# Kernel optimization log

Hardware: AMD Instinct MI355X
Metric: run time of the kernel (lower is better)

The kernel has to match this reference:

```python
import jax, jax.numpy as jnp
import numpy as np

N = 50000       # nodes
E = 1200000     # edges (before self-loops)
IN_CH = 128
HID = 64
L = 3           # FAConv layers
EPS_RES = 0.1   # FAConv eps residual weight
BN_EPS = 1e-5


def _bn(x, g, b):
    # BatchNorm1d, training-mode statistics (biased variance, like torch)
    mu = x.mean(axis=0)
    var = x.var(axis=0)
    return g * (x - mu) * jax.lax.rsqrt(var + BN_EPS) + b


def setup_inputs() -> dict:
    key = jax.random.key(0)
    ks = jax.random.split(key, 12)
    s = lambda d: 1.0 / np.sqrt(d)
    H2 = HID // 2
    return {
        "x": jax.random.normal(ks[0], (N, IN_CH), jnp.float32),
        "edge_index": jax.random.randint(ks[1], (2, E), 0, N, dtype=jnp.int32),
        "batch_size": 10000,
        "W_in": jax.random.normal(ks[2], (IN_CH, HID), jnp.float32) * s(IN_CH),
        "b_in": jnp.zeros((HID,), jnp.float32),
        "att_l": jax.random.normal(ks[3], (L, HID), jnp.float32) * s(HID),
        "att_r": jax.random.normal(ks[4], (L, HID), jnp.float32) * s(HID),
        "bn_g": jnp.ones((L, HID), jnp.float32),
        "bn_b": jnp.zeros((L, HID), jnp.float32),
        "W1": jax.random.normal(ks[5], (HID, HID), jnp.float32) * s(HID),
        "b1": jnp.zeros((HID,), jnp.float32),
        "g1": jnp.ones((HID,), jnp.float32),
        "be1": jnp.zeros((HID,), jnp.float32),
        "W2": jax.random.normal(ks[6], (HID, H2), jnp.float32) * s(HID),
        "b2": jnp.zeros((H2,), jnp.float32),
        "g2": jnp.ones((H2,), jnp.float32),
        "be2": jnp.zeros((H2,), jnp.float32),
        "W3": jax.random.normal(ks[7], (H2, 1), jnp.float32) * s(H2),
        "b3": jnp.zeros((1,), jnp.float32),
    }


def reference(x, edge_index, batch_size, W_in, b_in, att_l, att_r, bn_g, bn_b,
              W1, b1, g1, be1, W2, b2, g2, be2, W3, b3):
    n = x.shape[0]
    # gcn_norm with self-loops (same for all layers since graph is fixed)
    loops = jnp.arange(n, dtype=edge_index.dtype)
    src = jnp.concatenate([edge_index[0], loops])  # j (source)
    dst = jnp.concatenate([edge_index[1], loops])  # i (target)
    deg = jax.ops.segment_sum(jnp.ones_like(dst, dtype=x.dtype), dst, num_segments=n)
    dinv = jnp.where(deg > 0, jax.lax.rsqrt(deg), 0.0)
    norm = dinv[src] * dinv[dst]                   # [E+N]

    x0 = jax.nn.relu(x @ W_in + b_in)              # [N, HID]
    h = x0
    for l in range(L):
        al = h @ att_l[l]                          # [N] att_l^T x
        ar = h @ att_r[l]                          # [N] att_r^T x
        alpha = jnp.tanh(al[src] + ar[dst])        # [E+N] signed attention
        msg = h[src] * (alpha * norm)[:, None]     # gather + weight
        out = jax.ops.segment_sum(msg, dst, num_segments=n) + EPS_RES * x0
        h = _bn(jax.nn.relu(out), bn_g[l], bn_b[l])

    z = h[:batch_size]
    z = jax.nn.relu(_bn(z @ W1 + b1, g1, be1))
    z = jax.nn.relu(_bn(z @ W2 + b2, g2, be2))
    return (z @ W3 + b3).squeeze(-1)
```

## Files before the change

### kernel.cpp

```cpp
#include <hip/hip_runtime.h>
#include <hip/hip_bf16.h>
#include <math.h>

#define NND 50000
#define NE  1200000
#define TOT (NE + NND)
#define INCH 128
#define HID 64
#define H2  32
#define NL  3
#define BSZ 10000
#define NB  196
#define NHB 128
#define NSTAT 128
#define NAGG 2048
#define CHUNK 4096
#define EPS_RES 0.1f
#define BN_EPS 1e-5f

typedef unsigned short ushort8v __attribute__((ext_vector_type(8)));
typedef unsigned short ushort4v __attribute__((ext_vector_type(4)));

__device__ __forceinline__ float b2f(unsigned short u) {
    return __uint_as_float((unsigned)u << 16);
}

__device__ __forceinline__ float fast_tanh(float x) {
    float cx = fminf(fmaxf(x, -8.f), 8.f);
    float e = __expf(2.f * cx);
    return 1.f - __fdividef(2.f, e + 1.f);
}


__global__ __launch_bounds__(256) void bhist_kernel(const int* __restrict__ dst, int* __restrict__ bh_part, int ne) {
    __shared__ int arr[256];
    arr[threadIdx.x] = 0;
    __syncthreads();
    int i = blockIdx.x * 256 + threadIdx.x;
    int stride = gridDim.x * 256;
    for (int e = i; e < ne; e += stride) atomicAdd(&arr[dst[e] >> 8], 1);
    __syncthreads();
    bh_part[blockIdx.x * 256 + threadIdx.x] = arr[threadIdx.x];
}

__global__ __launch_bounds__(256) void bscan_kernel(const int* __restrict__ bh_part,
                                                    int* __restrict__ bstart, int* __restrict__ bcur,
                                                    int* __restrict__ offsets) {
    __shared__ int ls[256];
    int t = threadIdx.x;
    int v = 0;
    for (int k = 0; k < NHB; k++) v += bh_part[k * 256 + t];
    ls[t] = v;
    __syncthreads();
    for (int off = 1; off < 256; off <<= 1) {
        int tv = (t >= off) ? ls[t - off] : 0;
        __syncthreads();
        ls[t] += tv;
        __syncthreads();
    }
    int excl = ls[t] - v;
    if (t < NB) { bstart[t] = excl; bcur[t] = excl; }
    if (t == NB) bstart[NB] = ls[NB - 1];
    if (t == 0) offsets[NND] = TOT;
}

__global__ __launch_bounds__(256) void passA_kernel(const int* __restrict__ src, const int* __restrict__ dst,
                                                    int* __restrict__ bcur, unsigned* __restrict__ ebuf, int ne) {
    __shared__ int arr[256];
    int t = threadIdx.x;
    int base = blockIdx.x * CHUNK;
    int lim = min(base + CHUNK, ne);
    arr[t] = 0;
    __syncthreads();
    for (int e = base + t; e < lim; e += 256) atomicAdd(&arr[dst[e] >> 8], 1);
    __syncthreads();
    int cnt_t = arr[t];
    int claimed = 0;
    if (cnt_t > 0) claimed = atomicAdd(&bcur[t], cnt_t);
    __syncthreads();
    arr[t] = claimed;
    __syncthreads();
    for (int e = base + t; e < lim; e += 256) {
        int d = dst[e];
        int pos = atomicAdd(&arr[d >> 8], 1);
        ebuf[pos] = ((unsigned)src[e] << 8) | (unsigned)(d & 255);
    }
}

__global__ __launch_bounds__(256) void bucket_build_kernel(const unsigned* __restrict__ ebuf, const int* __restrict__ bstart,
                                                           int* __restrict__ offsets, int* __restrict__ csr,
                                                           float* __restrict__ aldi_f) {
    __shared__ int dcnt[256];
    __shared__ int ls[256];
    __shared__ int cur[256];
    int b = blockIdx.x, t = threadIdx.x;
    dcnt[t] = 0;
    __syncthreads();
    int beg = bstart[b], end = bstart[b + 1];
    for (int p = beg + t; p < end; p += 256) atomicAdd(&dcnt[ebuf[p] & 255u], 1);
    __syncthreads();
    int node = b * 256 + t;
    bool valid = node < NND;
    int d = valid ? (dcnt[t] + 1) : 0;
    ls[t] = d;
    __syncthreads();
    for (int off = 1; off < 256; off <<= 1) {
        int tv = (t >= off) ? ls[t - off] : 0;
        __syncthreads();
        ls[t] += tv;
        __syncthreads();
    }
    int off = bstart[b] + b * 256 + ls[t] - d;
    if (valid) {
        offsets[node] = off;
        aldi_f[2 * node + 1] = rsqrtf((float)d);
        csr[off] = node;
        cur[t] = off + 1;
    }
    __syncthreads();
    for (int p = beg + t; p < end; p += 256) {
        unsigned ed = ebuf[p];
        int pos = atomicAdd(&cur[ed & 255u], 1);
        csr[pos] = (int)(ed >> 8);
    }
}

__global__ __launch_bounds__(256) void gemm_in_kernel(const float* __restrict__ x, const float* __restrict__ W,
                                                      const float* __restrict__ b,
                                                      const float* __restrict__ attl, const float* __restrict__ attr,
                                                      __hip_bfloat16* __restrict__ x0bf,
                                                      float* __restrict__ aldi_f, float* __restrict__ ar) {
    __shared__ float Wl[INCH * HID];
    __shared__ float xs[16 * INCH];
    int t = threadIdx.x;
    for (int i = t; i < INCH * HID; i += 256) Wl[i] = W[i];
    size_t rowbase = (size_t)blockIdx.x * 16;
    for (int i = t; i < 16 * INCH; i += 256) xs[i] = x[rowbase * INCH + i];
    __syncthreads();
    int col = t & 63, rg = t >> 6;
    float a0 = 0.f, a1 = 0.f, a2 = 0.f, a3 = 0.f;
    for (int k = 0; k < INCH; k++) {
        float wk = Wl[k * HID + col];
        a0 = fmaf(xs[(rg * 4 + 0) * INCH + k], wk, a0);
        a1 = fmaf(xs[(rg * 4 + 1) * INCH + k], wk, a1);
        a2 = fmaf(xs[(rg * 4 + 2) * INCH + k], wk, a2);
        a3 = fmaf(xs[(rg * 4 + 3) * INCH + k], wk, a3);
    }
    float bb = b[col];
    a0 = fmaxf(a0 + bb, 0.f); a1 = fmaxf(a1 + bb, 0.f);
    a2 = fmaxf(a2 + bb, 0.f); a3 = fmaxf(a3 + bb, 0.f);
    size_t r = rowbase + rg * 4;
    x0bf[(r + 0) * HID + col] = __float2bfloat16(a0);
    x0bf[(r + 1) * HID + col] = __float2bfloat16(a1);
    x0bf[(r + 2) * HID + col] = __float2bfloat16(a2);
    x0bf[(r + 3) * HID + col] = __float2bfloat16(a3);
    float wl = attl[col], wr = attr[col];
    float p0 = a0 * wl, q0 = a0 * wr, p1 = a1 * wl, q1 = a1 * wr;
    float p2 = a2 * wl, q2 = a2 * wr, p3 = a3 * wl, q3 = a3 * wr;
    for (int off = 32; off > 0; off >>= 1) {
        p0 += __shfl_xor(p0, off); q0 += __shfl_xor(q0, off);
        p1 += __shfl_xor(p1, off); q1 += __shfl_xor(q1, off);
        p2 += __shfl_xor(p2, off); q2 += __shfl_xor(q2, off);
        p3 += __shfl_xor(p3, off); q3 += __shfl_xor(q3, off);
    }
    if (col == 0) {
        aldi_f[2 * (r + 0)] = p0; ar[r + 0] = q0;
        aldi_f[2 * (r + 1)] = p1; ar[r + 1] = q1;
        aldi_f[2 * (r + 2)] = p2; ar[r + 2] = q2;
        aldi_f[2 * (r + 3)] = p3; ar[r + 3] = q3;
    }
}

__global__ __launch_bounds__(256) void aggregate_kernel(const __hip_bfloat16* __restrict__ hbf,
                                                        const __hip_bfloat16* __restrict__ x0bf,
                                                        const float2* __restrict__ aldi,
                                                        const float* __restrict__ ar,
                                                        const int* __restrict__ offsets, const int* __restrict__ csr,
                                                        float* __restrict__ y, int n) {
    int wave = threadIdx.x >> 6;
    int lane = threadIdx.x & 63;
    int half = lane >> 5;
    int ll   = lane & 31;
    int sg   = ll >> 3;
    int cl   = (ll & 7) << 3;
    int hbase = half << 5;
    const unsigned short* hb = (const unsigned short*)hbf;
    for (int vb = blockIdx.x; (vb << 3) < n; vb += gridDim.x) {
        int v = (vb << 3) + (wave << 1) + half;
        bool vvalid = v < n;
        int beg = 0, end = 0;
        float arv = 0.f;
        if (vvalid) { beg = offsets[v]; end = offsets[v + 1]; arv = ar[v]; }
        int nstr = (end - beg + 31) >> 5;
        int mstr = max(nstr, __shfl_xor(nstr, 32));
        float a0 = 0.f, a1 = 0.f, a2 = 0.f, a3 = 0.f, a4 = 0.f, a5 = 0.f, a6 = 0.f, a7 = 0.f;
        for (int s = 0; s < mstr; ++s) {
            int sb = beg + (s << 5);
            int p = sb + ll;
            int u = 0; float c = 0.f;
            if (p < end) {
                u = csr[p];
                float2 ad = aldi[u];
                c = fast_tanh(ad.x + arv) * ad.y;
            }
            int cnt = end - sb;
            for (int ch = 0; ch < 2; ++ch) {
                int j0 = (ch << 4) + sg;
                int j1 = j0 + 4, j2 = j0 + 8, j3 = j0 + 12;
                int js0 = (j0 < cnt) ? j0 : 0;
                int js1 = (j1 < cnt) ? j1 : 0;
                int js2 = (j2 < cnt) ? j2 : 0;
                int js3 = (j3 < cnt) ? j3 : 0;
                int u0 = __shfl(u, hbase + js0); float c0 = __shfl(c, hbase + js0); if (j0 >= cnt) c0 = 0.f;
                int u1 = __shfl(u, hbase + js1); float c1 = __shfl(c, hbase + js1); if (j1 >= cnt) c1 = 0.f;
                int u2 = __shfl(u, hbase + js2); float c2 = __shfl(c, hbase + js2); if (j2 >= cnt) c2 = 0.f;
                int u3 = __shfl(u, hbase + js3); float c3 = __shfl(c, hbase + js3); if (j3 >= cnt) c3 = 0.f;
                ushort8v h0 = *(const ushort8v*)(hb + (size_t)u0 * HID + cl);
                ushort8v h1 = *(const ushort8v*)(hb + (size_t)u1 * HID + cl);
                ushort8v h2 = *(const ushort8v*)(hb + (size_t)u2 * HID + cl);
                ushort8v h3 = *(const ushort8v*)(hb + (size_t)u3 * HID + cl);
                a0 = fmaf(b2f(h0[0]), c0, a0); a1 = fmaf(b2f(h0[1]), c0, a1);
                a2 = fmaf(b2f(h0[2]), c0, a2); a3 = fmaf(b2f(h0[3]), c0, a3);
                a4 = fmaf(b2f(h0[4]), c0, a4); a5 = fmaf(b2f(h0[5]), c0, a5);
                a6 = fmaf(b2f(h0[6]), c0, a6); a7 = fmaf(b2f(h0[7]), c0, a7);
                a0 = fmaf(b2f(h1[0]), c1, a0); a1 = fmaf(b2f(h1[1]), c1, a1);
                a2 = fmaf(b2f(h1[2]), c1, a2); a3 = fmaf(b2f(h1[3]), c1, a3);
                a4 = fmaf(b2f(h1[4]), c1, a4); a5 = fmaf(b2f(h1[5]), c1, a5);
                a6 = fmaf(b2f(h1[6]), c1, a6); a7 = fmaf(b2f(h1[7]), c1, a7);
                a0 = fmaf(b2f(h2[0]), c2, a0); a1 = fmaf(b2f(h2[1]), c2, a1);
                a2 = fmaf(b2f(h2[2]), c2, a2); a3 = fmaf(b2f(h2[3]), c2, a3);
                a4 = fmaf(b2f(h2[4]), c2, a4); a5 = fmaf(b2f(h2[5]), c2, a5);
                a6 = fmaf(b2f(h2[6]), c2, a6); a7 = fmaf(b2f(h2[7]), c2, a7);
                a0 = fmaf(b2f(h3[0]), c3, a0); a1 = fmaf(b2f(h3[1]), c3, a1);
                a2 = fmaf(b2f(h3[2]), c3, a2); a3 = fmaf(b2f(h3[3]), c3, a3);
                a4 = fmaf(b2f(h3[4]), c3, a4); a5 = fmaf(b2f(h3[5]), c3, a5);
                a6 = fmaf(b2f(h3[6]), c3, a6); a7 = fmaf(b2f(h3[7]), c3, a7);
            }
        }
        for (int off = 8; off < 32; off <<= 1) {
            a0 += __shfl_xor(a0, off); a1 += __shfl_xor(a1, off);
            a2 += __shfl_xor(a2, off); a3 += __shfl_xor(a3, off);
            a4 += __shfl_xor(a4, off); a5 += __shfl_xor(a5, off);
            a6 += __shfl_xor(a6, off); a7 += __shfl_xor(a7, off);
        }
        if (sg == 0 && vvalid) {
            float dv = aldi[v].y;
            ushort8v xb = *(const ushort8v*)((const unsigned short*)x0bf + (size_t)v * HID + cl);
            float4 o0, o1;
            o0.x = fmaxf(fmaf(EPS_RES, b2f(xb[0]), a0 * dv), 0.f);
            o0.y = fmaxf(fmaf(EPS_RES, b2f(xb[1]), a1 * dv), 0.f);
            o0.z = fmaxf(fmaf(EPS_RES, b2f(xb[2]), a2 * dv), 0.f);
            o0.w = fmaxf(fmaf(EPS_RES, b2f(xb[3]), a3 * dv), 0.f);
            o1.x = fmaxf(fmaf(EPS_RES, b2f(xb[4]), a4 * dv), 0.f);
            o1.y = fmaxf(fmaf(EPS_RES, b2f(xb[5]), a5 * dv), 0.f);
            o1.z = fmaxf(fmaf(EPS_RES, b2f(xb[6]), a6 * dv), 0.f);
            o1.w = fmaxf(fmaf(EPS_RES, b2f(xb[7]), a7 * dv), 0.f);
            *(float4*)(y + (size_t)v * HID + cl) = o0;
            *(float4*)(y + (size_t)v * HID + cl + 4) = o1;
        }
    }
}

template <int C>
__global__ __launch_bounds__(256) void bn_stats_fused_kernel(const float* __restrict__ y, int rows,
                                                             const float* __restrict__ g, const float* __restrict__ b,
                                                             float rows_inv,
                                                             float* __restrict__ acc, int* __restrict__ counter,
                                                             float* __restrict__ scale, float* __restrict__ shift) {
    const int TPR = C / 4;
    const int RPW = 64 / TPR;
    int lane = threadIdx.x & 63;
    int wave = threadIdx.x >> 6;
    int cl = (lane % TPR) * 4;
    int rsub = lane / TPR;
    int rpb = 4 * RPW;
    int r = blockIdx.x * rpb + wave * RPW + rsub;
    int stride = gridDim.x * rpb;
    float s0 = 0.f, s1 = 0.f, s2 = 0.f, s3 = 0.f, q0 = 0.f, q1 = 0.f, q2 = 0.f, q3 = 0.f;
    for (; r < rows; r += stride) {
        float4 v = *(const float4*)(y + (size_t)r * C + cl);
        s0 += v.x; q0 = fmaf(v.x, v.x, q0);
        s1 += v.y; q1 = fmaf(v.y, v.y, q1);
        s2 += v.z; q2 = fmaf(v.z, v.z, q2);
        s3 += v.w; q3 = fmaf(v.w, v.w, q3);
    }
    for (int off = TPR; off < 64; off <<= 1) {
        s0 += __shfl_xor(s0, off); q0 += __shfl_xor(q0, off);
        s1 += __shfl_xor(s1, off); q1 += __shfl_xor(q1, off);
        s2 += __shfl_xor(s2, off); q2 += __shfl_xor(q2, off);
        s3 += __shfl_xor(s3, off); q3 += __shfl_xor(q3, off);
    }
    __shared__ float lsum[4][64], lsq[4][64];
    if (lane < TPR) {
        lsum[wave][cl + 0] = s0; lsq[wave][cl + 0] = q0;
        lsum[wave][cl + 1] = s1; lsq[wave][cl + 1] = q1;
        lsum[wave][cl + 2] = s2; lsq[wave][cl + 2] = q2;
        lsum[wave][cl + 3] = s3; lsq[wave][cl + 3] = q3;
    }
    __syncthreads();
    int t = threadIdx.x;
    if (t < C) {
        float ts = lsum[0][t] + lsum[1][t] + lsum[2][t] + lsum[3][t];
        float tq = lsq[0][t] + lsq[1][t] + lsq[2][t] + lsq[3][t];
        atomicAdd(&acc[t], ts);
        atomicAdd(&acc[64 + t], tq);
    }
    __shared__ int islast;
    __syncthreads();
    if (t == 0) {
        __threadfence();
        int old = atomicAdd(counter, 1);
        islast = (old == (int)gridDim.x - 1) ? 1 : 0;
    }
    __syncthreads();
    if (islast && t < C) {
        float ts = atomicAdd(&acc[t], 0.f);
        float tq = atomicAdd(&acc[64 + t], 0.f);
        float mean = ts * rows_inv;
        float var = tq * rows_inv - mean * mean;
        float sc = g[t] * rsqrtf(var + BN_EPS);
        scale[t] = sc;
        shift[t] = b[t] - mean * sc;
    }
}

__global__ __launch_bounds__(256) void bnapply_attn_kernel(const float* __restrict__ y, const float* __restrict__ scale,
                                                           const float* __restrict__ shift,
                                                           const float* __restrict__ attl, const float* __restrict__ attr,
                                                           __hip_bfloat16* __restrict__ hbf,
                                                           float* __restrict__ aldi_f, float* __restrict__ arr_out, int n) {
    int lane = threadIdx.x & 63;
    int wave = threadIdx.x >> 6;
    int rsub = lane >> 4;
    int cl = (lane & 15) << 2;
    int r = blockIdx.x * 16 + wave * 4 + rsub;
    if (r >= n) return;
    float4 v = *(const float4*)(y + (size_t)r * HID + cl);
    float4 sc = *(const float4*)(scale + cl);
    float4 sh = *(const float4*)(shift + cl);
    float v0 = fmaf(v.x, sc.x, sh.x);
    float v1 = fmaf(v.y, sc.y, sh.y);
    float v2 = fmaf(v.z, sc.z, sh.z);
    float v3 = fmaf(v.w, sc.w, sh.w);
    __hip_bfloat16 b0 = __float2bfloat16(v0), b1 = __float2bfloat16(v1);
    __hip_bfloat16 b2 = __float2bfloat16(v2), b3 = __float2bfloat16(v3);
    ushort4v hv;
    hv[0] = *(unsigned short*)&b0; hv[1] = *(unsigned short*)&b1;
    hv[2] = *(unsigned short*)&b2; hv[3] = *(unsigned short*)&b3;
    *(ushort4v*)((unsigned short*)hbf + (size_t)r * HID + cl) = hv;
    float4 wl4 = *(const float4*)(attl + cl);
    float4 wr4 = *(const float4*)(attr + cl);
    float pl = v0 * wl4.x + v1 * wl4.y + v2 * wl4.z + v3 * wl4.w;
    float pr = v0 * wr4.x + v1 * wr4.y + v2 * wr4.z + v3 * wr4.w;
    for (int off = 1; off < 16; off <<= 1) {
        pl += __shfl_xor(pl, off);
        pr += __shfl_xor(pr, off);
    }
    if ((lane & 15) == 0) { aldi_f[2 * r] = pl; arr_out[r] = pr; }
}

__global__ __launch_bounds__(256) void mlp1_kernel(const float* __restrict__ y, const float* __restrict__ scale,
                                                   const float* __restrict__ shift, const float* __restrict__ W,
                                                   const float* __restrict__ b, float* __restrict__ z1) {
    __shared__ float Wl[HID * HID];
    __shared__ float xs[16 * HID];
    int t = threadIdx.x;
    for (int i = t; i < HID * HID; i += 256) Wl[i] = W[i];
    size_t rowbase = (size_t)blockIdx.x * 16;
    for (int i = t; i < 16 * HID; i += 256) {
        int c = i & 63;
        xs[i] = fmaf(y[rowbase * HID + i], scale[c], shift[c]);
    }
    __syncthreads();
    int col = t & 63, rg = t >> 6;
    float a0 = 0.f, a1 = 0.f, a2 = 0.f, a3 = 0.f;
    for (int k = 0; k < HID; k++) {
        float wk = Wl[k * HID + col];
        a0 = fmaf(xs[(rg * 4 + 0) * HID + k], wk, a0);
        a1 = fmaf(xs[(rg * 4 + 1) * HID + k], wk, a1);
        a2 = fmaf(xs[(rg * 4 + 2) * HID + k], wk, a2);
        a3 = fmaf(xs[(rg * 4 + 3) * HID + k], wk, a3);
    }
    float bb = b[col];
    size_t r = rowbase + rg * 4;
    z1[(r + 0) * HID + col] = a0 + bb;
    z1[(r + 1) * HID + col] = a1 + bb;
    z1[(r + 2) * HID + col] = a2 + bb;
    z1[(r + 3) * HID + col] = a3 + bb;
}

__global__ __launch_bounds__(256) void mlp2_kernel(const float* __restrict__ z1, const float* __restrict__ scale,
                                                   const float* __restrict__ shift, const float* __restrict__ W,
                                                   const float* __restrict__ b, float* __restrict__ z2) {
    __shared__ float Wl[HID * H2];
    __shared__ float as[16 * HID];
    int t = threadIdx.x;
    for (int i = t; i < HID * H2; i += 256) Wl[i] = W[i];
    size_t rowbase = (size_t)blockIdx.x * 16;
    for (int i = t; i < 16 * HID; i += 256) {
        int c = i & 63;
        float v = z1[rowbase * HID + i];
        as[i] = fmaxf(fmaf(v, scale[c], shift[c]), 0.f);
    }
    __syncthreads();
    int col = t & 31, rg = t >> 5;
    float a0 = 0.f, a1 = 0.f;
    for (int k = 0; k < HID; k++) {
        float wk = Wl[k * H2 + col];
        a0 = fmaf(as[(rg * 2 + 0) * HID + k], wk, a0);
        a1 = fmaf(as[(rg * 2 + 1) * HID + k], wk, a1);
    }
    float bb = b[col];
    size_t r = rowbase + rg * 2;
    z2[(r + 0) * H2 + col] = a0 + bb;
    z2[(r + 1) * H2 + col] = a1 + bb;
}

__global__ __launch_bounds__(256) void mlp3_kernel(const float* __restrict__ z2, const float* __restrict__ scale,
                                                   const float* __restrict__ shift, const float* __restrict__ W3,
                                                   const float* __restrict__ b3, float* __restrict__ out, int rows) {
    int i = blockIdx.x * 256 + threadIdx.x;
    if (i >= rows) return;
    float acc = 0.f;
#pragma unroll
    for (int k = 0; k < H2; k++) {
        float v = fmaxf(fmaf(z2[(size_t)i * H2 + k], scale[k], shift[k]), 0.f);
        acc = fmaf(v, W3[k], acc);
    }
    out[i] = acc + b3[0];
}

extern "C" void kernel_launch(void* const* d_in, const int* in_sizes, int n_in,
                              void* d_out, int out_size, void* d_ws, size_t ws_size,
                              hipStream_t stream) {
    const float* x     = (const float*)d_in[0];
    const int*   ei    = (const int*)d_in[1];
    const int*   src   = ei;
    const int*   dst   = ei + NE;
    const float* W_in  = (const float*)d_in[3];
    const float* b_in  = (const float*)d_in[4];
    const float* att_l = (const float*)d_in[5];
    const float* att_r = (const float*)d_in[6];
    const float* bn_g  = (const float*)d_in[7];
    const float* bn_b  = (const float*)d_in[8];
    const float* W1    = (const float*)d_in[9];
    const float* b1    = (const float*)d_in[10];
    const float* g1    = (const float*)d_in[11];
    const float* be1   = (const float*)d_in[12];
    const float* W2    = (const float*)d_in[13];
    const float* b2    = (const float*)d_in[14];
    const float* g2    = (const float*)d_in[15];
    const float* be2   = (const float*)d_in[16];
    const float* W3    = (const float*)d_in[17];
    const float* b3    = (const float*)d_in[18];
    float* out = (float*)d_out;

    char* p = (char*)d_ws;
    auto carve = [&](size_t bytes) -> void* {
        void* r = (void*)p;
        p += (bytes + 255) & ~(size_t)255;
        return r;
    };
    int*   bh_part = (int*)carve((size_t)NHB * 256 * 4);
    int*   bstart  = (int*)carve(256 * 4);
    int*   bcur    = (int*)carve(256 * 4);
    int*   offsets = (int*)carve((size_t)(NND + 1) * 4);
    int*   csr     = (int*)carve((size_t)TOT * 4);
    float2* aldi   = (float2*)carve((size_t)NND * 8);
    float* ar      = (float*)carve((size_t)NND * 4);
    __hip_bfloat16* x0bf = (__hip_bfloat16*)carve((size_t)NND * HID * 2);
    __hip_bfloat16* hbfA = (__hip_bfloat16*)carve((size_t)NND * HID * 2);
    __hip_bfloat16* hbfB = (__hip_bfloat16*)carve((size_t)NND * HID * 2);
    float* ybuf    = (float*)carve((size_t)NND * HID * 4);
    unsigned* ebuf = (unsigned*)ybuf;
    float* accall  = (float*)carve(5 * 256 * 4);
    float* scale   = (float*)carve(64 * 4);
    float* shift   = (float*)carve(64 * 4);
    float* z1      = (float*)carve((size_t)BSZ * HID * 4);
    float* z2      = (float*)carve((size_t)BSZ * H2 * 4);

    auto accr = [&](int i) -> float* { return accall + i * 256; };
    auto ctr  = [&](int i) -> int*   { return (int*)(accall + i * 256 + 128); };

    const int nblkA = (NE + CHUNK - 1) / CHUNK;

    hipMemsetAsync(accall, 0, 5 * 256 * 4, stream);

    bhist_kernel<<<NHB, 256, 0, stream>>>(dst, bh_part, NE);
    gemm_in_kernel<<<NND / 16, 256, 0, stream>>>(x, W_in, b_in, att_l, att_r, x0bf, (float*)aldi, ar);
    bscan_kernel<<<1, 256, 0, stream>>>(bh_part, bstart, bcur, offsets);
    passA_kernel<<<nblkA, 256, 0, stream>>>(src, dst, bcur, ebuf, NE);
    bucket_build_kernel<<<NB, 256, 0, stream>>>(ebuf, bstart, offsets, csr, (float*)aldi);

    const __hip_bfloat16* h_in = x0bf;
    __hip_bfloat16* hbufs[2] = {hbfA, hbfB};
    for (int l = 0; l < NL; l++) {
        aggregate_kernel<<<NAGG, 256, 0, stream>>>(h_in, x0bf, aldi, ar, offsets, csr, ybuf, NND);
        bn_stats_fused_kernel<64><<<NSTAT, 256, 0, stream>>>(ybuf, NND, bn_g + l * HID, bn_b + l * HID,
                                                             1.0f / NND, accr(l), ctr(l), scale, shift);
        if (l < NL - 1) {
            bnapply_attn_kernel<<<(NND + 15) / 16, 256, 0, stream>>>(ybuf, scale, shift,
                                                                     att_l + (l + 1) * HID, att_r + (l + 1) * HID,
                                                                     hbufs[l], (float*)aldi, ar, NND);
            h_in = hbufs[l];
        }
    }

    mlp1_kernel<<<BSZ / 16, 256, 0, stream>>>(ybuf, scale, shift, W1, b1, z1);
    bn_stats_fused_kernel<64><<<NSTAT, 256, 0, stream>>>(z1, BSZ, g1, be1, 1.0f / BSZ, accr(3), ctr(3), scale, shift);

    mlp2_kernel<<<BSZ / 16, 256, 0, stream>>>(z1, scale, shift, W2, b2, z2);
    bn_stats_fused_kernel<32><<<NSTAT, 256, 0, stream>>>(z2, BSZ, g2, be2, 1.0f / BSZ, accr(4), ctr(4), scale, shift);

    mlp3_kernel<<<(BSZ + 255) / 256, 256, 0, stream>>>(z2, scale, shift, W3, b3, out, BSZ);
}
```

Before: 347.9 us.

## Fuse histogram scan into bhist and BN statistics into MLP kernels

Merges the bucket-scan kernel into the histogram kernel: global atomics accumulate the histogram and a last-block-done counter lets the final block run the scan. It also drops the two separate BN-statistics launches in the head MLP. Each MLP GEMM kernel now accumulates column sums and sums of squares with atomics, and the next kernel derives scale and shift from them. This removes three kernel launches and one re-read of z1 and z2, at the cost of global atomic contention and less precise E[x^2]-mean^2 variance.

New measurement: 357.6 us. 1.03x slower.

```diff
diff --git a/kernel.cpp b/kernel.cpp
--- a/kernel.cpp
+++ b/kernel.cpp
@@ -32,24 +32,30 @@
 }
 
 
-__global__ __launch_bounds__(256) void bhist_kernel(const int* __restrict__ dst, int* __restrict__ bh_part, int ne) {
+__global__ __launch_bounds__(256) void bhist_kernel(const int* __restrict__ dst, int* __restrict__ ghist,
+                                                    int* __restrict__ counter,
+                                                    int* __restrict__ bstart, int* __restrict__ bcur,
+                                                    int* __restrict__ offsets, int ne) {
     __shared__ int arr[256];
-    arr[threadIdx.x] = 0;
-    __syncthreads();
-    int i = blockIdx.x * 256 + threadIdx.x;
+    int t = threadIdx.x;
+    arr[t] = 0;
+    __syncthreads();
+    int i = blockIdx.x * 256 + t;
     int stride = gridDim.x * 256;
     for (int e = i; e < ne; e += stride) atomicAdd(&arr[dst[e] >> 8], 1);
     __syncthreads();
-    bh_part[blockIdx.x * 256 + threadIdx.x] = arr[threadIdx.x];
-}
-
-__global__ __launch_bounds__(256) void bscan_kernel(const int* __restrict__ bh_part,
-                                                    int* __restrict__ bstart, int* __restrict__ bcur,
-                                                    int* __restrict__ offsets) {
+    if (arr[t] > 0) atomicAdd(&ghist[t], arr[t]);
+    __shared__ int islast;
+    __syncthreads();
+    if (t == 0) {
+        __threadfence();
+        int old = atomicAdd(counter, 1);
+        islast = (old == (int)gridDim.x - 1) ? 1 : 0;
+    }
+    __syncthreads();
+    if (!islast) return;
     __shared__ int ls[256];
-    int t = threadIdx.x;
-    int v = 0;
-    for (int k = 0; k < NHB; k++) v += bh_part[k * 256 + t];
+    int v = atomicAdd(&ghist[t], 0);
     ls[t] = v;
     __syncthreads();
     for (int off = 1; off < 256; off <<= 1) {
@@ -361,9 +367,11 @@
 
 __global__ __launch_bounds__(256) void mlp1_kernel(const float* __restrict__ y, const float* __restrict__ scale,
                                                    const float* __restrict__ shift, const float* __restrict__ W,
-                                                   const float* __restrict__ b, float* __restrict__ z1) {
+                                                   const float* __restrict__ b, float* __restrict__ z1,
+                                                   float* __restrict__ acc_out) {
     __shared__ float Wl[HID * HID];
     __shared__ float xs[16 * HID];
+    __shared__ float zs[4][64], zq[4][64];
     int t = threadIdx.x;
     for (int i = t; i < HID * HID; i += 256) Wl[i] = W[i];
     size_t rowbase = (size_t)blockIdx.x * 16;
@@ -382,25 +390,48 @@
         a3 = fmaf(xs[(rg * 4 + 3) * HID + k], wk, a3);
     }
     float bb = b[col];
+    a0 += bb; a1 += bb; a2 += bb; a3 += bb;
     size_t r = rowbase + rg * 4;
-    z1[(r + 0) * HID + col] = a0 + bb;
-    z1[(r + 1) * HID + col] = a1 + bb;
-    z1[(r + 2) * HID + col] = a2 + bb;
-    z1[(r + 3) * HID + col] = a3 + bb;
-}
-
-__global__ __launch_bounds__(256) void mlp2_kernel(const float* __restrict__ z1, const float* __restrict__ scale,
-                                                   const float* __restrict__ shift, const float* __restrict__ W,
-                                                   const float* __restrict__ b, float* __restrict__ z2) {
+    z1[(r + 0) * HID + col] = a0;
+    z1[(r + 1) * HID + col] = a1;
+    z1[(r + 2) * HID + col] = a2;
+    z1[(r + 3) * HID + col] = a3;
+    zs[rg][col] = a0 + a1 + a2 + a3;
+    zq[rg][col] = a0 * a0 + a1 * a1 + a2 * a2 + a3 * a3;
+    __syncthreads();
+    if (t < 64) {
+        float s = zs[0][t] + zs[1][t] + zs[2][t] + zs[3][t];
+        float q = zq[0][t] + zq[1][t] + zq[2][t] + zq[3][t];
+        atomicAdd(&acc_out[t], s);
+        atomicAdd(&acc_out[64 + t], q);
+    }
+}
+
+__global__ __launch_bounds__(256) void mlp2_kernel(const float* __restrict__ z1,
+                                                   const float* __restrict__ acc_in, float rows_inv_in,
+                                                   const float* __restrict__ gin, const float* __restrict__ bin,
+                                                   const float* __restrict__ W, const float* __restrict__ b,
+                                                   float* __restrict__ z2, float* __restrict__ acc_out) {
     __shared__ float Wl[HID * H2];
     __shared__ float as[16 * HID];
-    int t = threadIdx.x;
+    __shared__ float s_sc[64], s_sh[64];
+    __shared__ float zs[8][32], zq[8][32];
+    int t = threadIdx.x;
+    if (t < 64) {
+        float ts = acc_in[t], tq = acc_in[64 + t];
+        float mean = ts * rows_inv_in;
+        float var = tq * rows_inv_in - mean * mean;
+        float sc = gin[t] * rsqrtf(var + BN_EPS);
+        s_sc[t] = sc;
+        s_sh[t] = bin[t] - mean * sc;
+    }
     for (int i = t; i < HID * H2; i += 256) Wl[i] = W[i];
+    __syncthreads();
     size_t rowbase = (size_t)blockIdx.x * 16;
     for (int i = t; i < 16 * HID; i += 256) {
         int c = i & 63;
         float v = z1[rowbase * HID + i];
-        as[i] = fmaxf(fmaf(v, scale[c], shift[c]), 0.f);
+        as[i] = fmaxf(fmaf(v, s_sc[c], s_sh[c]), 0.f);
     }
     __syncthreads();
     int col = t & 31, rg = t >> 5;
@@ -411,20 +442,44 @@
         a1 = fmaf(as[(rg * 2 + 1) * HID + k], wk, a1);
     }
     float bb = b[col];
+    a0 += bb; a1 += bb;
     size_t r = rowbase + rg * 2;
-    z2[(r + 0) * H2 + col] = a0 + bb;
-    z2[(r + 1) * H2 + col] = a1 + bb;
-}
-
-__global__ __launch_bounds__(256) void mlp3_kernel(const float* __restrict__ z2, const float* __restrict__ scale,
-                                                   const float* __restrict__ shift, const float* __restrict__ W3,
-                                                   const float* __restrict__ b3, float* __restrict__ out, int rows) {
-    int i = blockIdx.x * 256 + threadIdx.x;
+    z2[(r + 0) * H2 + col] = a0;
+    z2[(r + 1) * H2 + col] = a1;
+    zs[rg][col] = a0 + a1;
+    zq[rg][col] = a0 * a0 + a1 * a1;
+    __syncthreads();
+    if (t < 32) {
+        float s = 0.f, q = 0.f;
+#pragma unroll
+        for (int w = 0; w < 8; w++) { s += zs[w][t]; q += zq[w][t]; }
+        atomicAdd(&acc_out[t], s);
+        atomicAdd(&acc_out[64 + t], q);
+    }
+}
+
+__global__ __launch_bounds__(256) void mlp3_kernel(const float* __restrict__ z2,
+                                                   const float* __restrict__ acc_in, float rows_inv_in,
+                                                   const float* __restrict__ gin, const float* __restrict__ bin,
+                                                   const float* __restrict__ W3, const float* __restrict__ b3,
+                                                   float* __restrict__ out, int rows) {
+    __shared__ float s_sc[32], s_sh[32];
+    int t = threadIdx.x;
+    if (t < 32) {
+        float ts = acc_in[t], tq = acc_in[64 + t];
+        float mean = ts * rows_inv_in;
+        float var = tq * rows_inv_in - mean * mean;
+        float sc = gin[t] * rsqrtf(var + BN_EPS);
+        s_sc[t] = sc;
+        s_sh[t] = bin[t] - mean * sc;
+    }
+    __syncthreads();
+    int i = blockIdx.x * 256 + t;
     if (i >= rows) return;
     float acc = 0.f;
 #pragma unroll
     for (int k = 0; k < H2; k++) {
-        float v = fmaxf(fmaf(z2[(size_t)i * H2 + k], scale[k], shift[k]), 0.f);
+        float v = fmaxf(fmaf(z2[(size_t)i * H2 + k], s_sc[k], s_sh[k]), 0.f);
         acc = fmaf(v, W3[k], acc);
     }
     out[i] = acc + b3[0];
@@ -461,7 +516,6 @@
         p += (bytes + 255) & ~(size_t)255;
         return r;
     };
-    int*   bh_part = (int*)carve((size_t)NHB * 256 * 4);
     int*   bstart  = (int*)carve(256 * 4);
     int*   bcur    = (int*)carve(256 * 4);
     int*   offsets = (int*)carve((size_t)(NND + 1) * 4);
@@ -473,7 +527,7 @@
     __hip_bfloat16* hbfB = (__hip_bfloat16*)carve((size_t)NND * HID * 2);
     float* ybuf    = (float*)carve((size_t)NND * HID * 4);
     unsigned* ebuf = (unsigned*)ybuf;
-    float* accall  = (float*)carve(5 * 256 * 4);
+    float* accall  = (float*)carve(7 * 256 * 4);
     float* scale   = (float*)carve(64 * 4);
     float* shift   = (float*)carve(64 * 4);
     float* z1      = (float*)carve((size_t)BSZ * HID * 4);
@@ -481,14 +535,15 @@
 
     auto accr = [&](int i) -> float* { return accall + i * 256; };
     auto ctr  = [&](int i) -> int*   { return (int*)(accall + i * 256 + 128); };
+    int* ghist    = (int*)(accall + 5 * 256);
+    int* ghctr    = (int*)(accall + 6 * 256);
 
     const int nblkA = (NE + CHUNK - 1) / CHUNK;
 
-    hipMemsetAsync(accall, 0, 5 * 256 * 4, stream);
-
-    bhist_kernel<<<NHB, 256, 0, stream>>>(dst, bh_part, NE);
+    hipMemsetAsync(accall, 0, 7 * 256 * 4, stream);
+
+    bhist_kernel<<<NHB, 256, 0, stream>>>(dst, ghist, ghctr, bstart, bcur, offsets, NE);
     gemm_in_kernel<<<NND / 16, 256, 0, stream>>>(x, W_in, b_in, att_l, att_r, x0bf, (float*)aldi, ar);
-    bscan_kernel<<<1, 256, 0, stream>>>(bh_part, bstart, bcur, offsets);
     passA_kernel<<<nblkA, 256, 0, stream>>>(src, dst, bcur, ebuf, NE);
     bucket_build_kernel<<<NB, 256, 0, stream>>>(ebuf, bstart, offsets, csr, (float*)aldi);
 
@@ -506,11 +561,7 @@
         }
     }
 
-    mlp1_kernel<<<BSZ / 16, 256, 0, stream>>>(ybuf, scale, shift, W1, b1, z1);
-    bn_stats_fused_kernel<64><<<NSTAT, 256, 0, stream>>>(z1, BSZ, g1, be1, 1.0f / BSZ, accr(3), ctr(3), scale, shift);
-
-    mlp2_kernel<<<BSZ / 16, 256, 0, stream>>>(z1, scale, shift, W2, b2, z2);
-    bn_stats_fused_kernel<32><<<NSTAT, 256, 0, stream>>>(z2, BSZ, g2, be2, 1.0f / BSZ, accr(4), ctr(4), scale, shift);
-
-    mlp3_kernel<<<(BSZ + 255) / 256, 256, 0, stream>>>(z2, scale, shift, W3, b3, out, BSZ);
-}
+    mlp1_kernel<<<BSZ / 16, 256, 0, stream>>>(ybuf, scale, shift, W1, b1, z1, accr(3));
+    mlp2_kernel<<<BSZ / 16, 256, 0, stream>>>(z1, accr(3), 1.0f / BSZ, g1, be1, W2, b2, z2, accr(4));
+    mlp3_kernel<<<(BSZ + 255) / 256, 256, 0, stream>>>(z2, accr(4), 1.0f / BSZ, g2, be2, W3, b3, out, BSZ);
+}
```

## Split input GEMM over K across waves with weights held in registers

Applied to the files above, without the earlier changes.

The input projection kernel no longer stages the full 128x64 weight matrix and the x tile in shared memory. Each wave now keeps a 32-row K-slice of W in registers, reads x rows directly with wave-uniform float4 loads, and computes partial dot products for all 16 rows. The four partials are then reduced through a small shared buffer. This removes the 32KB shared staging and its LDS traffic per block, at the cost of more registers and a cross-wave reduction step.

After: 346.9 us. About the same (-0.3%).

```diff
diff --git a/kernel.cpp b/kernel.cpp
--- a/kernel.cpp
+++ b/kernel.cpp
@@ -130,22 +130,39 @@
                                                       const float* __restrict__ attl, const float* __restrict__ attr,
                                                       __hip_bfloat16* __restrict__ x0bf,
                                                       float* __restrict__ aldi_f, float* __restrict__ ar) {
-    __shared__ float Wl[INCH * HID];
-    __shared__ float xs[16 * INCH];
+    __shared__ float part[4][16][64];
     int t = threadIdx.x;
-    for (int i = t; i < INCH * HID; i += 256) Wl[i] = W[i];
+    int lane = t & 63;
+    int wq = __builtin_amdgcn_readfirstlane(t >> 6);
     size_t rowbase = (size_t)blockIdx.x * 16;
-    for (int i = t; i < 16 * INCH; i += 256) xs[i] = x[rowbase * INCH + i];
-    __syncthreads();
-    int col = t & 63, rg = t >> 6;
-    float a0 = 0.f, a1 = 0.f, a2 = 0.f, a3 = 0.f;
-    for (int k = 0; k < INCH; k++) {
-        float wk = Wl[k * HID + col];
-        a0 = fmaf(xs[(rg * 4 + 0) * INCH + k], wk, a0);
-        a1 = fmaf(xs[(rg * 4 + 1) * INCH + k], wk, a1);
-        a2 = fmaf(xs[(rg * 4 + 2) * INCH + k], wk, a2);
-        a3 = fmaf(xs[(rg * 4 + 3) * INCH + k], wk, a3);
-    }
+    float wreg[32];
+#pragma unroll
+    for (int kk = 0; kk < 32; kk++)
+        wreg[kk] = W[(size_t)(wq * 32 + kk) * HID + lane];
+    const float* xbase = x + rowbase * INCH + wq * 32;
+#pragma unroll
+    for (int r = 0; r < 16; r++) {
+        const float4* xr = (const float4*)(xbase + (size_t)r * INCH);
+        float4 v0 = xr[0], v1 = xr[1], v2 = xr[2], v3 = xr[3];
+        float4 v4 = xr[4], v5 = xr[5], v6 = xr[6], v7 = xr[7];
+        float s = 0.f;
+        s = fmaf(v0.x, wreg[ 0], s); s = fmaf(v0.y, wreg[ 1], s); s = fmaf(v0.z, wreg[ 2], s); s = fmaf(v0.w, wreg[ 3], s);
+        s = fmaf(v1.x, wreg[ 4], s); s = fmaf(v1.y, wreg[ 5], s); s = fmaf(v1.z, wreg[ 6], s); s = fmaf(v1.w, wreg[ 7], s);
+        s = fmaf(v2.x, wreg[ 8], s); s = fmaf(v2.y, wreg[ 9], s); s = fmaf(v2.z, wreg[10], s); s = fmaf(v2.w, wreg[11], s);
+        s = fmaf(v3.x, wreg[12], s); s = fmaf(v3.y, wreg[13], s); s = fmaf(v3.z, wreg[14], s); s = fmaf(v3.w, wreg[15], s);
+        s = fmaf(v4.x, wreg[16], s); s = fmaf(v4.y, wreg[17], s); s = fmaf(v4.z, wreg[18], s); s = fmaf(v4.w, wreg[19], s);
+        s = fmaf(v5.x, wreg[20], s); s = fmaf(v5.y, wreg[21], s); s = fmaf(v5.z, wreg[22], s); s = fmaf(v5.w, wreg[23], s);
+        s = fmaf(v6.x, wreg[24], s); s = fmaf(v6.y, wreg[25], s); s = fmaf(v6.z, wreg[26], s); s = fmaf(v6.w, wreg[27], s);
+        s = fmaf(v7.x, wreg[28], s); s = fmaf(v7.y, wreg[29], s); s = fmaf(v7.z, wreg[30], s); s = fmaf(v7.w, wreg[31], s);
+        part[wq][r][lane] = s;
+    }
+    __syncthreads();
+    int col = lane, rg = t >> 6;
+    int r0 = rg * 4;
+    float a0 = part[0][r0 + 0][col] + part[1][r0 + 0][col] + part[2][r0 + 0][col] + part[3][r0 + 0][col];
+    float a1 = part[0][r0 + 1][col] + part[1][r0 + 1][col] + part[2][r0 + 1][col] + part[3][r0 + 1][col];
+    float a2 = part[0][r0 + 2][col] + part[1][r0 + 2][col] + part[2][r0 + 2][col] + part[3][r0 + 2][col];
+    float a3 = part[0][r0 + 3][col] + part[1][r0 + 3][col] + part[2][r0 + 3][col] + part[3][r0 + 3][col];
     float bb = b[col];
     a0 = fmaxf(a0 + bb, 0.f); a1 = fmaxf(a1 + bb, 0.f);
     a2 = fmaxf(a2 + bb, 0.f); a3 = fmaxf(a3 + bb, 0.f);
```
